# Kernel optimization log

Measured on AMD Instinct MI355X. Metric: run time of the kernel, lower is better.

Reference implementation:

```python
import jax, jax.numpy as jnp
import numpy as np

B, S, T = 256, 1024, 128

def setup_inputs() -> dict:
    key = jax.random.key(0)
    k1, k2, k3, k4, k5 = jax.random.split(key, 5)
    return {
        "emissions": jax.random.normal(k1, (B, S, T), dtype=jnp.float32),
        "tags": jax.random.randint(k2, (B, S), 0, T, dtype=jnp.int64 if jax.config.jax_enable_x64 else jnp.int32),
        "mask": jnp.ones((B, S), dtype=jnp.float32),
        "start_transitions": jax.random.normal(k3, (T,), dtype=jnp.float32),
        "end_transitions": jax.random.normal(k4, (T,), dtype=jnp.float32),
        "transitions": jax.random.normal(k5, (T, T), dtype=jnp.float32),
    }


def _gold_score(emissions, tags, mask, start_transitions, end_transitions, transitions):
    # score of the gold tag sequence (note: original uses log_softmax'd emissions here)
    score = start_transitions[tags[:, 0]]
    logp = jax.nn.log_softmax(emissions, axis=2)
    em_sc = jnp.take_along_axis(logp, tags[:, :, None], axis=2)[:, :, 0] * mask  # [B,S]
    score = score + em_sc.sum(axis=1)
    trans_sc = transitions[tags[:, :-1], tags[:, 1:]] * mask[:, 1:]  # [B,S-1]
    score = score + trans_sc.sum(axis=1)
    score = score + end_transitions[tags[:, -1]] * mask[:, -1]
    return score


def _forward_score(emissions, mask, start_transitions, end_transitions, transitions):
    # partition function via forward algorithm (faithful to original, incl. its
    # masking quirk: alpha recurrence is unmasked; only the last step's masked
    # alpha is used for the final logsumexp)
    alpha0 = start_transitions + emissions[:, 0]  # [B,T]

    def step(carry, inp):
        alpha, _ = carry
        em_t, m_t = inp  # [B,T], [B]
        # [B,T_prev,T_cur] broadcast add, logsumexp over prev tag
        new_alpha = jax.nn.logsumexp(
            alpha[:, :, None] + transitions[None, :, :] + em_t[:, None, :], axis=1
        )
        return (new_alpha, new_alpha * m_t[:, None]), None

    xs = (jnp.swapaxes(emissions[:, 1:], 0, 1), jnp.swapaxes(mask[:, 1:], 0, 1))
    (_, alpha_masked), _ = jax.lax.scan(step, (alpha0, jnp.zeros_like(alpha0)), xs)
    return jax.nn.logsumexp(alpha_masked + end_transitions, axis=1)  # [B]


def reference(emissions, tags, mask, start_transitions, end_transitions, transitions):
    score = _gold_score(emissions, tags, mask, start_transitions, end_transitions, transitions)
    fwd = _forward_score(emissions, mask, start_transitions, end_transitions, transitions)
    return jnp.mean(fwd - score)
```

## Files before the change

kernel.cpp:

```cpp
#include <hip/hip_runtime.h>

#define CRF_B 256
#define CRF_S 1024
#define CRF_T 128
#define GSPLIT 8
#define NFWD   CRF_B
#define NGOLD  (CRF_B * GSPLIT)
#define WS_FWD (CRF_B * GSPLIT)
#define WS_N   (WS_FWD + CRF_B)

typedef __attribute__((ext_vector_type(4))) float f32x4;

__device__ __forceinline__ void barrier_lds_only() {
    __asm__ volatile("s_waitcnt lgkmcnt(0)\n\ts_barrier" ::: "memory");
}

__device__ __forceinline__ float dpp_add_xor1(float x) {
    int y = __builtin_amdgcn_mov_dpp(__float_as_int(x), 0xB1, 0xF, 0xF, false);
    return x + __int_as_float(y);
}
__device__ __forceinline__ float dpp_add_xor2(float x) {
    int y = __builtin_amdgcn_mov_dpp(__float_as_int(x), 0x4E, 0xF, 0xF, false);
    return x + __int_as_float(y);
}

__device__ __forceinline__ f32x4 exp4(f32x4 v) {
    f32x4 r;
    r.x = __expf(v.x); r.y = __expf(v.y); r.z = __expf(v.z); r.w = __expf(v.w);
    return r;
}
__device__ __forceinline__ float hsum4(f32x4 v) {
    return (v.x + v.y) + (v.z + v.w);
}

__device__ __forceinline__ void fwd_block(
    const int b, const int tid,
    const float* __restrict__ em, const float* __restrict__ mask,
    const float* __restrict__ startT, const float* __restrict__ endT,
    const float* __restrict__ trans, float* __restrict__ ws)
{
    const int r  = tid & 3;
    const int cq = tid >> 2;
    const int j0 = cq * 4;
    const bool leader = (r == 0);

    __shared__ __align__(16) float Abuf[2][CRF_T];
    __shared__ __align__(16) float partsA[32];
    __shared__ float red[4];
    __shared__ float lzsh;

    int kidx[8];
#pragma unroll
    for (int k = 0; k < 8; ++k) kidx[k] = (k + 2 * r) & 7;

    f32x4 EE[8][4];
#pragma unroll
    for (int k = 0; k < 8; ++k) {
#pragma unroll
        for (int s = 0; s < 4; ++s) {
            const int i = 32 * r + 4 * kidx[k] + s;
            f32x4 t4 = *(const f32x4*)&trans[i * CRF_T + j0];
            EE[k][0][s] = __expf(t4.x);
            EE[k][1][s] = __expf(t4.y);
            EE[k][2][s] = __expf(t4.z);
            EE[k][3][s] = __expf(t4.w);
        }
    }

    const float* emb = em + (size_t)b * CRF_S * CRF_T + j0;
    const float mlast = mask[(size_t)b * CRF_S + (CRF_S - 1)];

    float logZ = 0.f;
    float rc = 1.f;

    f32x4 emv[4], eh[2][4];
#pragma unroll
    for (int k = 0; k < 4; ++k) emv[k] = *(const f32x4*)(emb + (size_t)k * CRF_T);
#pragma unroll
    for (int k = 0; k < 4; ++k) eh[0][k] = exp4(emv[k]);
#pragma unroll
    for (int k = 0; k < 4; ++k) emv[k] = *(const f32x4*)(emb + (size_t)(4 + k) * CRF_T);

    auto STEP = [&](int t, int role, f32x4 ehv) {
        const int rb = (t & 1) ^ 1, wb = t & 1;

        if (role == 3 && leader && t < 1023) {
            const f32x4* pa = (const f32x4*)partsA;
            f32x4 s8 = ((pa[0] + pa[1]) + (pa[2] + pa[3])) +
                       ((pa[4] + pa[5]) + (pa[6] + pa[7]));
            float c = hsum4(s8);
            rc = __builtin_amdgcn_rcpf(c);
            logZ += __logf(c);
        }

        const f32x4* A4 = (const f32x4*)&Abuf[rb][32 * r];
        f32x4 av = A4[kidx[0]];
        f32x4 ac0 = av * EE[0][0];
        f32x4 ac1 = av * EE[0][1];
        f32x4 ac2 = av * EE[0][2];
        f32x4 ac3 = av * EE[0][3];
#pragma unroll
        for (int k = 1; k < 8; ++k) {
            av = A4[kidx[k]];
            ac0 = __builtin_elementwise_fma(av, EE[k][0], ac0);
            ac1 = __builtin_elementwise_fma(av, EE[k][1], ac1);
            ac2 = __builtin_elementwise_fma(av, EE[k][2], ac2);
            ac3 = __builtin_elementwise_fma(av, EE[k][3], ac3);
        }
        float d0 = hsum4(ac0), d1 = hsum4(ac1), d2 = hsum4(ac2), d3 = hsum4(ac3);
        d0 = dpp_add_xor2(dpp_add_xor1(d0));
        d1 = dpp_add_xor2(dpp_add_xor1(d1));
        d2 = dpp_add_xor2(dpp_add_xor1(d2));
        d3 = dpp_add_xor2(dpp_add_xor1(d3));

        float a0 = d0 * ehv.x, a1 = d1 * ehv.y, a2 = d2 * ehv.z, a3 = d3 * ehv.w;
        if (role == 0) { a0 *= rc; a1 *= rc; a2 *= rc; a3 *= rc; }
        if (leader) {
            f32x4 avw = {a0, a1, a2, a3};
            *(f32x4*)&Abuf[wb][j0] = avw;
            if (role == 2) partsA[cq] = (a0 + a1) + (a2 + a3);
        }
        barrier_lds_only();
    };

    {
        f32x4 s4 = *(const f32x4*)&startT[j0];
        if (leader) {
            f32x4 a;
            a.x = __expf(s4.x) * eh[0][0].x;
            a.y = __expf(s4.y) * eh[0][0].y;
            a.z = __expf(s4.z) * eh[0][0].z;
            a.w = __expf(s4.w) * eh[0][0].w;
            *(f32x4*)&Abuf[0][j0] = a;
        }
        barrier_lds_only();
        STEP(1, 1, eh[0][1]);
#pragma unroll
        for (int k = 0; k < 4; ++k) eh[1][k] = exp4(emv[k]);
        STEP(2, 2, eh[0][2]);
#pragma unroll
        for (int k = 0; k < 4; ++k) emv[k] = *(const f32x4*)(emb + (size_t)(8 + k) * CRF_T);
        STEP(3, 3, eh[0][3]);
    }

#pragma unroll 1
    for (int g = 1; g < 256; ++g) {
        const int t0 = 4 * g;
        const int cur = g & 1, nxt = cur ^ 1;
        STEP(t0 + 0, 0, eh[cur][0]);
        STEP(t0 + 1, 1, eh[cur][1]);
        if (g <= 254) {
#pragma unroll
            for (int k = 0; k < 4; ++k) eh[nxt][k] = exp4(emv[k]);
        }
        STEP(t0 + 2, 2, eh[cur][2]);
        if (g <= 253) {
#pragma unroll
            for (int k = 0; k < 4; ++k)
                emv[k] = *(const f32x4*)(emb + (size_t)(t0 + 8 + k) * CRF_T);
        }
        STEP(t0 + 3, 3, eh[cur][3]);
    }

    __syncthreads();
    if (tid == 0) lzsh = logZ;
    __syncthreads();
    const float lz = lzsh;

    float v = (__logf(Abuf[1][tid]) + lz) * mlast + endT[tid];
    float mx = v;
#pragma unroll
    for (int dd = 1; dd < 64; dd <<= 1) mx = fmaxf(mx, __shfl_xor(mx, dd));
    if ((tid & 63) == 0) red[tid >> 6] = mx;
    __syncthreads();
    mx = fmaxf(red[0], red[1]);
    float ex = __expf(v - mx);
#pragma unroll
    for (int dd = 1; dd < 64; dd <<= 1) ex += __shfl_xor(ex, dd);
    if ((tid & 63) == 0) red[2 + (tid >> 6)] = ex;
    __syncthreads();
    if (tid == 0)
        ws[WS_FWD + b] = mx + __logf(red[2] + red[3]);
}

__device__ __forceinline__ void gold_block(
    const int gb, const int tid,
    const float* __restrict__ em, const int* __restrict__ tags,
    const float* __restrict__ mask, const float* __restrict__ startT,
    const float* __restrict__ endT, const float* __restrict__ trans,
    float* __restrict__ ws)
{
    const int b     = gb >> 3;
    const int slice = gb & (GSPLIT - 1);
    const int base  = slice << 7;
    const int p = tid & 3;
    const int q = tid >> 2;
    const int* tg = tags + (size_t)b * CRF_S;
    const float* mk = mask + (size_t)b * CRF_S;
    const float* emr = em + (size_t)b * CRF_S * CRF_T;

    __shared__ float r2g[2];

    float g_acc = 0.f;
    {
        const int t = base + tid;
        const int tagt = tg[t];
        const float m = mk[t];
        g_acc += emr[(size_t)t * CRF_T + tagt] * m;
        if (t >= 1) g_acc += trans[tg[t - 1] * CRF_T + tagt] * m;
    }
    if (tid == 0 && slice == 0)
        g_acc += startT[tg[0]];
    if (tid == 0 && slice == GSPLIT - 1)
        g_acc += endT[tg[CRF_S - 1]] * mk[CRF_S - 1];

    float s2 = 0.f;
#pragma unroll
    for (int it = 0; it < 4; ++it) {
        const int rr = base + it * 32 + q;
        const float* row = emr + (size_t)rr * CRF_T;
        f32x4 sum4 = {0.f, 0.f, 0.f, 0.f};
#pragma unroll
        for (int k = 0; k < 8; ++k)
            sum4 += exp4(*(const f32x4*)(row + k * 16 + p * 4));
        float s = hsum4(sum4);
        s = dpp_add_xor1(s);
        s = dpp_add_xor2(s);
        if (p == 0) s2 += __logf(s) * mk[rr];
    }

    float contrib = s2 - g_acc;
#pragma unroll
    for (int d = 1; d < 64; d <<= 1) contrib += __shfl_xor(contrib, d);
    if ((tid & 63) == 0) r2g[tid >> 6] = contrib;
    __syncthreads();
    if (tid == 0)
        ws[gb] = r2g[0] + r2g[1];
}

__global__ __launch_bounds__(128, 1) void crf_main_kernel(
    const float* __restrict__ em, const int* __restrict__ tags,
    const float* __restrict__ mask, const float* __restrict__ startT,
    const float* __restrict__ endT, const float* __restrict__ trans,
    float* __restrict__ ws)
{
    if (blockIdx.x < NFWD)
        fwd_block(blockIdx.x, threadIdx.x, em, mask, startT, endT, trans, ws);
    else
        gold_block(blockIdx.x - NFWD, threadIdx.x, em, tags, mask, startT,
                   endT, trans, ws);
}

__global__ __launch_bounds__(256) void crf_reduce_kernel(
    const float* __restrict__ ws, float* __restrict__ out)
{
    const int tid = threadIdx.x;
    float s = 0.f;
#pragma unroll
    for (int k = 0; k < WS_N; k += 256) s += ws[k + tid];
#pragma unroll
    for (int d = 1; d < 64; d <<= 1) s += __shfl_xor(s, d);
    __shared__ float r4[4];
    if ((tid & 63) == 0) r4[tid >> 6] = s;
    __syncthreads();
    if (tid == 0)
        out[0] = ((r4[0] + r4[1]) + (r4[2] + r4[3])) * (1.0f / CRF_B);
}

extern "C" void kernel_launch(void* const* d_in, const int* in_sizes, int n_in,
                              void* d_out, int out_size, void* d_ws, size_t ws_size,
                              hipStream_t stream)
{
    const float* em     = (const float*)d_in[0];
    const int*   tags   = (const int*)d_in[1];
    const float* mask   = (const float*)d_in[2];
    const float* startT = (const float*)d_in[3];
    const float* endT   = (const float*)d_in[4];
    const float* trans  = (const float*)d_in[5];
    float* out = (float*)d_out;
    float* ws  = (float*)d_ws;

    hipLaunchKernelGGL(crf_main_kernel, dim3(NFWD + NGOLD), dim3(128), 0, stream,
                       em, tags, mask, startT, endT, trans, ws);
    hipLaunchKernelGGL(crf_reduce_kernel, dim3(1), dim3(256), 0, stream,
                       ws, out);
}
```

Measured before the change: 597.1 us.

## Run CRF forward recurrence in a single wave, replacing barriers with permlane swaps

The forward-algorithm block now uses only one 64-lane wavefront instead of two. Each half-wave covers 64 of the 128 previous tags and combines its partial sums with permlane32_swap, so the per-step s_barrier is gone. The normalizer is recomputed by every lane from the LDS alpha vector, and the final logsumexp stays in registers without shared reductions. The cost is twice as many exp-transition registers per thread (16x4 f32x4) and more FMA work per lane, which puts register pressure and occupancy at risk. Correctness also depends on LDS ordering within one wave without explicit barriers.

```diff
diff --git a/kernel.cpp b/kernel.cpp
--- a/kernel.cpp
+++ b/kernel.cpp
@@ -11,8 +11,14 @@
 
 typedef __attribute__((ext_vector_type(4))) float f32x4;
 
-__device__ __forceinline__ void barrier_lds_only() {
-    __asm__ volatile("s_waitcnt lgkmcnt(0)\n\ts_barrier" ::: "memory");
+__device__ __forceinline__ void wait_lds() {
+    __asm__ volatile("s_waitcnt lgkmcnt(0)" ::: "memory");
+}
+
+__device__ __forceinline__ float xhalf_sum(float x) {
+    int xi = __float_as_int(x);
+    auto r = __builtin_amdgcn_permlane32_swap(xi, xi, false, false);
+    return __int_as_float(r[0]) + __int_as_float(r[1]);
 }
 
 __device__ __forceinline__ float dpp_add_xor1(float x) {
@@ -39,31 +45,23 @@
     const float* __restrict__ startT, const float* __restrict__ endT,
     const float* __restrict__ trans, float* __restrict__ ws)
 {
-    const int r  = tid & 3;
-    const int cq = tid >> 2;
-    const int j0 = cq * 4;
-    const bool leader = (r == 0);
-
-    __shared__ __align__(16) float Abuf[2][CRF_T];
-    __shared__ __align__(16) float partsA[32];
-    __shared__ float red[4];
-    __shared__ float lzsh;
-
-    int kidx[8];
-#pragma unroll
-    for (int k = 0; k < 8; ++k) kidx[k] = (k + 2 * r) & 7;
-
-    f32x4 EE[8][4];
-#pragma unroll
-    for (int k = 0; k < 8; ++k) {
+    __shared__ __align__(16) float Ab[2][CRF_T];
+
+    const int h  = tid >> 5;
+    const int c  = tid & 31;
+    const int j0 = 4 * c;
+
+    f32x4 EH[16][4];
+#pragma unroll
+    for (int k = 0; k < 16; ++k) {
 #pragma unroll
         for (int s = 0; s < 4; ++s) {
-            const int i = 32 * r + 4 * kidx[k] + s;
-            f32x4 t4 = *(const f32x4*)&trans[i * CRF_T + j0];
-            EE[k][0][s] = __expf(t4.x);
-            EE[k][1][s] = __expf(t4.y);
-            EE[k][2][s] = __expf(t4.z);
-            EE[k][3][s] = __expf(t4.w);
+            const int row = 64 * h + 4 * k + s;
+            f32x4 t4 = *(const f32x4*)&trans[row * CRF_T + j0];
+            EH[k][0][s] = __expf(t4.x);
+            EH[k][1][s] = __expf(t4.y);
+            EH[k][2][s] = __expf(t4.z);
+            EH[k][3][s] = __expf(t4.w);
         }
     }
 
@@ -72,6 +70,7 @@
 
     float logZ = 0.f;
     float rc = 1.f;
+    f32x4 aout = {0.f, 0.f, 0.f, 0.f};
 
     f32x4 emv[4], eh[2][4];
 #pragma unroll
@@ -84,56 +83,59 @@
     auto STEP = [&](int t, int role, f32x4 ehv) {
         const int rb = (t & 1) ^ 1, wb = t & 1;
 
-        if (role == 3 && leader && t < 1023) {
-            const f32x4* pa = (const f32x4*)partsA;
-            f32x4 s8 = ((pa[0] + pa[1]) + (pa[2] + pa[3])) +
-                       ((pa[4] + pa[5]) + (pa[6] + pa[7]));
-            float c = hsum4(s8);
-            rc = __builtin_amdgcn_rcpf(c);
-            logZ += __logf(c);
-        }
-
-        const f32x4* A4 = (const f32x4*)&Abuf[rb][32 * r];
-        f32x4 av = A4[kidx[0]];
-        f32x4 ac0 = av * EE[0][0];
-        f32x4 ac1 = av * EE[0][1];
-        f32x4 ac2 = av * EE[0][2];
-        f32x4 ac3 = av * EE[0][3];
-#pragma unroll
-        for (int k = 1; k < 8; ++k) {
-            av = A4[kidx[k]];
-            ac0 = __builtin_elementwise_fma(av, EE[k][0], ac0);
-            ac1 = __builtin_elementwise_fma(av, EE[k][1], ac1);
-            ac2 = __builtin_elementwise_fma(av, EE[k][2], ac2);
-            ac3 = __builtin_elementwise_fma(av, EE[k][3], ac3);
-        }
-        float d0 = hsum4(ac0), d1 = hsum4(ac1), d2 = hsum4(ac2), d3 = hsum4(ac3);
-        d0 = dpp_add_xor2(dpp_add_xor1(d0));
-        d1 = dpp_add_xor2(dpp_add_xor1(d1));
-        d2 = dpp_add_xor2(dpp_add_xor1(d2));
-        d3 = dpp_add_xor2(dpp_add_xor1(d3));
-
-        float a0 = d0 * ehv.x, a1 = d1 * ehv.y, a2 = d2 * ehv.z, a3 = d3 * ehv.w;
-        if (role == 0) { a0 *= rc; a1 *= rc; a2 *= rc; a3 *= rc; }
-        if (leader) {
-            f32x4 avw = {a0, a1, a2, a3};
-            *(f32x4*)&Abuf[wb][j0] = avw;
-            if (role == 2) partsA[cq] = (a0 + a1) + (a2 + a3);
-        }
-        barrier_lds_only();
+        wait_lds();
+
+        const f32x4* A4 = (const f32x4*)&Ab[rb][64 * h];
+        f32x4 av[16];
+#pragma unroll
+        for (int k = 0; k < 16; ++k) av[k] = A4[k];
+
+        if (role == 3 && t < 1023) {
+            f32x4 cs = ((av[0] + av[1]) + (av[2] + av[3])) +
+                       ((av[4] + av[5]) + (av[6] + av[7]));
+            cs += ((av[8] + av[9]) + (av[10] + av[11])) +
+                  ((av[12] + av[13]) + (av[14] + av[15]));
+            float ch = hsum4(cs);
+            float cfull = xhalf_sum(ch);
+            rc = __builtin_amdgcn_rcpf(cfull);
+            logZ += __logf(cfull);
+        }
+
+        f32x4 ac0 = av[0] * EH[0][0];
+        f32x4 ac1 = av[0] * EH[0][1];
+        f32x4 ac2 = av[0] * EH[0][2];
+        f32x4 ac3 = av[0] * EH[0][3];
+#pragma unroll
+        for (int k = 1; k < 16; ++k) {
+            ac0 = __builtin_elementwise_fma(av[k], EH[k][0], ac0);
+            ac1 = __builtin_elementwise_fma(av[k], EH[k][1], ac1);
+            ac2 = __builtin_elementwise_fma(av[k], EH[k][2], ac2);
+            ac3 = __builtin_elementwise_fma(av[k], EH[k][3], ac3);
+        }
+        float d0 = xhalf_sum(hsum4(ac0));
+        float d1 = xhalf_sum(hsum4(ac1));
+        float d2 = xhalf_sum(hsum4(ac2));
+        float d3 = xhalf_sum(hsum4(ac3));
+
+        f32x4 a4;
+        a4.x = d0 * ehv.x; a4.y = d1 * ehv.y;
+        a4.z = d2 * ehv.z; a4.w = d3 * ehv.w;
+        if (role == 0) { a4.x *= rc; a4.y *= rc; a4.z *= rc; a4.w *= rc; }
+        if (h == 0)
+            *(f32x4*)&Ab[wb][j0] = a4;
+        aout = a4;
     };
 
     {
         f32x4 s4 = *(const f32x4*)&startT[j0];
-        if (leader) {
-            f32x4 a;
-            a.x = __expf(s4.x) * eh[0][0].x;
-            a.y = __expf(s4.y) * eh[0][0].y;
-            a.z = __expf(s4.z) * eh[0][0].z;
-            a.w = __expf(s4.w) * eh[0][0].w;
-            *(f32x4*)&Abuf[0][j0] = a;
-        }
-        barrier_lds_only();
+        f32x4 a;
+        a.x = __expf(s4.x) * eh[0][0].x;
+        a.y = __expf(s4.y) * eh[0][0].y;
+        a.z = __expf(s4.z) * eh[0][0].z;
+        a.w = __expf(s4.w) * eh[0][0].w;
+        if (h == 0)
+            *(f32x4*)&Ab[0][j0] = a;
+        aout = a;
         STEP(1, 1, eh[0][1]);
 #pragma unroll
         for (int k = 0; k < 4; ++k) eh[1][k] = exp4(emv[k]);
@@ -162,25 +164,22 @@
         STEP(t0 + 3, 3, eh[cur][3]);
     }
 
-    __syncthreads();
-    if (tid == 0) lzsh = logZ;
-    __syncthreads();
-    const float lz = lzsh;
-
-    float v = (__logf(Abuf[1][tid]) + lz) * mlast + endT[tid];
-    float mx = v;
-#pragma unroll
-    for (int dd = 1; dd < 64; dd <<= 1) mx = fmaxf(mx, __shfl_xor(mx, dd));
-    if ((tid & 63) == 0) red[tid >> 6] = mx;
-    __syncthreads();
-    mx = fmaxf(red[0], red[1]);
-    float ex = __expf(v - mx);
-#pragma unroll
-    for (int dd = 1; dd < 64; dd <<= 1) ex += __shfl_xor(ex, dd);
-    if ((tid & 63) == 0) red[2 + (tid >> 6)] = ex;
-    __syncthreads();
+    f32x4 v4;
+    v4.x = (__logf(aout.x) + logZ) * mlast + endT[j0 + 0];
+    v4.y = (__logf(aout.y) + logZ) * mlast + endT[j0 + 1];
+    v4.z = (__logf(aout.z) + logZ) * mlast + endT[j0 + 2];
+    v4.w = (__logf(aout.w) + logZ) * mlast + endT[j0 + 3];
+    float mx = fmaxf(fmaxf(v4.x, v4.y), fmaxf(v4.z, v4.w));
+#pragma unroll
+    for (int d = 1; d < 64; d <<= 1) mx = fmaxf(mx, __shfl_xor(mx, d));
+    float ex = 0.f;
+    if (h == 0)
+        ex = __expf(v4.x - mx) + __expf(v4.y - mx) +
+             __expf(v4.z - mx) + __expf(v4.w - mx);
+#pragma unroll
+    for (int d = 1; d < 64; d <<= 1) ex += __shfl_xor(ex, d);
     if (tid == 0)
-        ws[WS_FWD + b] = mx + __logf(red[2] + red[3]);
+        ws[WS_FWD + b] = mx + __logf(ex);
 }
 
 __device__ __forceinline__ void gold_block(
@@ -244,11 +243,13 @@
     const float* __restrict__ endT, const float* __restrict__ trans,
     float* __restrict__ ws)
 {
-    if (blockIdx.x < NFWD)
+    if (blockIdx.x < NFWD) {
+        if (threadIdx.x >= 64) return;
         fwd_block(blockIdx.x, threadIdx.x, em, mask, startT, endT, trans, ws);
-    else
+    } else {
         gold_block(blockIdx.x - NFWD, threadIdx.x, em, tags, mask, startT,
                    endT, trans, ws);
+    }
 }
 
 __global__ __launch_bounds__(256) void crf_reduce_kernel(
```

Result: slower. 1.088 ms (+82.2%).

## Widen CRF blocks to 256 threads and fuse final reduction via atomic counter

Applied to the files above, without the earlier changes.

The forward recurrence now spreads each column's reduction over previous tags across 8 lanes instead of 4. That halves the per-thread FMA chain on the serial critical path, at the cost of one extra DPP reduction stage. The four LDS reads for a step are issued first, before the prefetch and exp work, to hide their latency. The separate reduce kernel is removed: the last block, found by an atomic counter, does the final sum, with a memset to reset the counter. Gold blocks are adapted to 256 threads. The wider blocks give each CU more active waves but also more barrier participants per step.

```diff
diff --git a/kernel.cpp b/kernel.cpp
--- a/kernel.cpp
+++ b/kernel.cpp
@@ -6,6 +6,7 @@
 #define GSPLIT 8
 #define NFWD   CRF_B
 #define NGOLD  (CRF_B * GSPLIT)
+#define NBLK   (NFWD + NGOLD)
 #define WS_FWD (CRF_B * GSPLIT)
 #define WS_N   (WS_FWD + CRF_B)
 
@@ -21,6 +22,10 @@
 }
 __device__ __forceinline__ float dpp_add_xor2(float x) {
     int y = __builtin_amdgcn_mov_dpp(__float_as_int(x), 0x4E, 0xF, 0xF, false);
+    return x + __int_as_float(y);
+}
+__device__ __forceinline__ float dpp_add_xor4u(float x) {
+    int y = __builtin_amdgcn_mov_dpp(__float_as_int(x), 0x141, 0xF, 0xF, false);
     return x + __int_as_float(y);
 }
 
@@ -39,26 +44,26 @@
     const float* __restrict__ startT, const float* __restrict__ endT,
     const float* __restrict__ trans, float* __restrict__ ws)
 {
-    const int r  = tid & 3;
-    const int cq = tid >> 2;
+    const int r = tid & 7;
+    const int cq = tid >> 3;
     const int j0 = cq * 4;
     const bool leader = (r == 0);
 
     __shared__ __align__(16) float Abuf[2][CRF_T];
     __shared__ __align__(16) float partsA[32];
-    __shared__ float red[4];
+    __shared__ float red[8];
     __shared__ float lzsh;
 
-    int kidx[8];
-#pragma unroll
-    for (int k = 0; k < 8; ++k) kidx[k] = (k + 2 * r) & 7;
-
-    f32x4 EE[8][4];
-#pragma unroll
-    for (int k = 0; k < 8; ++k) {
+    int kidx[4];
+#pragma unroll
+    for (int k = 0; k < 4; ++k) kidx[k] = (k + r) & 3;
+
+    f32x4 EE[4][4];
+#pragma unroll
+    for (int k = 0; k < 4; ++k) {
 #pragma unroll
         for (int s = 0; s < 4; ++s) {
-            const int i = 32 * r + 4 * kidx[k] + s;
+            const int i = r * 16 + kidx[k] * 4 + s;
             f32x4 t4 = *(const f32x4*)&trans[i * CRF_T + j0];
             EE[k][0][s] = __expf(t4.x);
             EE[k][1][s] = __expf(t4.y);
@@ -81,8 +86,15 @@
 #pragma unroll
     for (int k = 0; k < 4; ++k) emv[k] = *(const f32x4*)(emb + (size_t)(4 + k) * CRF_T);
 
-    auto STEP = [&](int t, int role, f32x4 ehv) {
+    auto STEP = [&](int t, int role, f32x4 ehv, auto&& filler) {
         const int rb = (t & 1) ^ 1, wb = t & 1;
+
+        const f32x4* A4 = (const f32x4*)&Abuf[rb][r * 16];
+        f32x4 av[4];
+#pragma unroll
+        for (int k = 0; k < 4; ++k) av[k] = A4[kidx[k]];
+
+        filler();
 
         if (role == 3 && leader && t < 1023) {
             const f32x4* pa = (const f32x4*)partsA;
@@ -93,25 +105,22 @@
             logZ += __logf(c);
         }
 
-        const f32x4* A4 = (const f32x4*)&Abuf[rb][32 * r];
-        f32x4 av = A4[kidx[0]];
-        f32x4 ac0 = av * EE[0][0];
-        f32x4 ac1 = av * EE[0][1];
-        f32x4 ac2 = av * EE[0][2];
-        f32x4 ac3 = av * EE[0][3];
-#pragma unroll
-        for (int k = 1; k < 8; ++k) {
-            av = A4[kidx[k]];
-            ac0 = __builtin_elementwise_fma(av, EE[k][0], ac0);
-            ac1 = __builtin_elementwise_fma(av, EE[k][1], ac1);
-            ac2 = __builtin_elementwise_fma(av, EE[k][2], ac2);
-            ac3 = __builtin_elementwise_fma(av, EE[k][3], ac3);
+        f32x4 ac0 = av[0] * EE[0][0];
+        f32x4 ac1 = av[0] * EE[0][1];
+        f32x4 ac2 = av[0] * EE[0][2];
+        f32x4 ac3 = av[0] * EE[0][3];
+#pragma unroll
+        for (int k = 1; k < 4; ++k) {
+            ac0 = __builtin_elementwise_fma(av[k], EE[k][0], ac0);
+            ac1 = __builtin_elementwise_fma(av[k], EE[k][1], ac1);
+            ac2 = __builtin_elementwise_fma(av[k], EE[k][2], ac2);
+            ac3 = __builtin_elementwise_fma(av[k], EE[k][3], ac3);
         }
         float d0 = hsum4(ac0), d1 = hsum4(ac1), d2 = hsum4(ac2), d3 = hsum4(ac3);
-        d0 = dpp_add_xor2(dpp_add_xor1(d0));
-        d1 = dpp_add_xor2(dpp_add_xor1(d1));
-        d2 = dpp_add_xor2(dpp_add_xor1(d2));
-        d3 = dpp_add_xor2(dpp_add_xor1(d3));
+        d0 = dpp_add_xor4u(dpp_add_xor2(dpp_add_xor1(d0)));
+        d1 = dpp_add_xor4u(dpp_add_xor2(dpp_add_xor1(d1)));
+        d2 = dpp_add_xor4u(dpp_add_xor2(dpp_add_xor1(d2)));
+        d3 = dpp_add_xor4u(dpp_add_xor2(dpp_add_xor1(d3)));
 
         float a0 = d0 * ehv.x, a1 = d1 * ehv.y, a2 = d2 * ehv.z, a3 = d3 * ehv.w;
         if (role == 0) { a0 *= rc; a1 *= rc; a2 *= rc; a3 *= rc; }
@@ -122,6 +131,8 @@
         }
         barrier_lds_only();
     };
+
+    auto NOFILL = [] {};
 
     {
         f32x4 s4 = *(const f32x4*)&startT[j0];
@@ -134,32 +145,37 @@
             *(f32x4*)&Abuf[0][j0] = a;
         }
         barrier_lds_only();
-        STEP(1, 1, eh[0][1]);
-#pragma unroll
-        for (int k = 0; k < 4; ++k) eh[1][k] = exp4(emv[k]);
-        STEP(2, 2, eh[0][2]);
-#pragma unroll
-        for (int k = 0; k < 4; ++k) emv[k] = *(const f32x4*)(emb + (size_t)(8 + k) * CRF_T);
-        STEP(3, 3, eh[0][3]);
+        STEP(1, 1, eh[0][1], NOFILL);
+        STEP(2, 2, eh[0][2], [&] {
+#pragma unroll
+            for (int k = 0; k < 4; ++k) eh[1][k] = exp4(emv[k]);
+        });
+        STEP(3, 3, eh[0][3], [&] {
+#pragma unroll
+            for (int k = 0; k < 4; ++k)
+                emv[k] = *(const f32x4*)(emb + (size_t)(8 + k) * CRF_T);
+        });
     }
 
 #pragma unroll 1
     for (int g = 1; g < 256; ++g) {
         const int t0 = 4 * g;
         const int cur = g & 1, nxt = cur ^ 1;
-        STEP(t0 + 0, 0, eh[cur][0]);
-        STEP(t0 + 1, 1, eh[cur][1]);
-        if (g <= 254) {
-#pragma unroll
-            for (int k = 0; k < 4; ++k) eh[nxt][k] = exp4(emv[k]);
-        }
-        STEP(t0 + 2, 2, eh[cur][2]);
-        if (g <= 253) {
-#pragma unroll
-            for (int k = 0; k < 4; ++k)
-                emv[k] = *(const f32x4*)(emb + (size_t)(t0 + 8 + k) * CRF_T);
-        }
-        STEP(t0 + 3, 3, eh[cur][3]);
+        STEP(t0 + 0, 0, eh[cur][0], NOFILL);
+        STEP(t0 + 1, 1, eh[cur][1], NOFILL);
+        STEP(t0 + 2, 2, eh[cur][2], [&] {
+            if (g <= 254) {
+#pragma unroll
+                for (int k = 0; k < 4; ++k) eh[nxt][k] = exp4(emv[k]);
+            }
+        });
+        STEP(t0 + 3, 3, eh[cur][3], [&] {
+            if (g <= 253) {
+#pragma unroll
+                for (int k = 0; k < 4; ++k)
+                    emv[k] = *(const f32x4*)(emb + (size_t)(t0 + 8 + k) * CRF_T);
+            }
+        });
     }
 
     __syncthreads();
@@ -167,20 +183,22 @@
     __syncthreads();
     const float lz = lzsh;
 
-    float v = (__logf(Abuf[1][tid]) + lz) * mlast + endT[tid];
+    float v = -3.0e38f;
+    if (tid < 128)
+        v = (__logf(Abuf[1][tid]) + lz) * mlast + endT[tid];
     float mx = v;
 #pragma unroll
     for (int dd = 1; dd < 64; dd <<= 1) mx = fmaxf(mx, __shfl_xor(mx, dd));
     if ((tid & 63) == 0) red[tid >> 6] = mx;
     __syncthreads();
-    mx = fmaxf(red[0], red[1]);
-    float ex = __expf(v - mx);
+    mx = fmaxf(fmaxf(red[0], red[1]), fmaxf(red[2], red[3]));
+    float ex = (tid < 128) ? __expf(v - mx) : 0.f;
 #pragma unroll
     for (int dd = 1; dd < 64; dd <<= 1) ex += __shfl_xor(ex, dd);
-    if ((tid & 63) == 0) red[2 + (tid >> 6)] = ex;
+    if ((tid & 63) == 0) red[4 + (tid >> 6)] = ex;
     __syncthreads();
     if (tid == 0)
-        ws[WS_FWD + b] = mx + __logf(red[2] + red[3]);
+        ws[WS_FWD + b] = mx + __logf((red[4] + red[5]) + (red[6] + red[7]));
 }
 
 __device__ __forceinline__ void gold_block(
@@ -199,10 +217,10 @@
     const float* mk = mask + (size_t)b * CRF_S;
     const float* emr = em + (size_t)b * CRF_S * CRF_T;
 
-    __shared__ float r2g[2];
+    __shared__ float r4g[4];
 
     float g_acc = 0.f;
-    {
+    if (tid < 128) {
         const int t = base + tid;
         const int tagt = tg[t];
         const float m = mk[t];
@@ -216,8 +234,8 @@
 
     float s2 = 0.f;
 #pragma unroll
-    for (int it = 0; it < 4; ++it) {
-        const int rr = base + it * 32 + q;
+    for (int it = 0; it < 2; ++it) {
+        const int rr = base + it * 64 + q;
         const float* row = emr + (size_t)rr * CRF_T;
         f32x4 sum4 = {0.f, 0.f, 0.f, 0.f};
 #pragma unroll
@@ -232,39 +250,47 @@
     float contrib = s2 - g_acc;
 #pragma unroll
     for (int d = 1; d < 64; d <<= 1) contrib += __shfl_xor(contrib, d);
-    if ((tid & 63) == 0) r2g[tid >> 6] = contrib;
+    if ((tid & 63) == 0) r4g[tid >> 6] = contrib;
     __syncthreads();
     if (tid == 0)
-        ws[gb] = r2g[0] + r2g[1];
-}
-
-__global__ __launch_bounds__(128, 1) void crf_main_kernel(
+        ws[gb] = (r4g[0] + r4g[1]) + (r4g[2] + r4g[3]);
+}
+
+__device__ __forceinline__ void finish_and_reduce(
+    float* __restrict__ ws, float* __restrict__ out, const int tid)
+{
+    __shared__ unsigned osh;
+    __shared__ float r4f[4];
+    __threadfence();
+    if (tid == 0)
+        osh = atomicAdd((unsigned*)(ws + WS_N), 1u);
+    __syncthreads();
+    if (osh != (unsigned)(NBLK - 1)) return;
+    __threadfence();
+
+    float s = 0.f;
+#pragma unroll
+    for (int k = 0; k < WS_N; k += 256) s += ws[k + tid];
+#pragma unroll
+    for (int d = 1; d < 64; d <<= 1) s += __shfl_xor(s, d);
+    if ((tid & 63) == 0) r4f[tid >> 6] = s;
+    __syncthreads();
+    if (tid == 0)
+        out[0] = ((r4f[0] + r4f[1]) + (r4f[2] + r4f[3])) * (1.0f / CRF_B);
+}
+
+__global__ __launch_bounds__(256) void crf_main_kernel(
     const float* __restrict__ em, const int* __restrict__ tags,
     const float* __restrict__ mask, const float* __restrict__ startT,
     const float* __restrict__ endT, const float* __restrict__ trans,
-    float* __restrict__ ws)
+    float* __restrict__ ws, float* __restrict__ out)
 {
     if (blockIdx.x < NFWD)
         fwd_block(blockIdx.x, threadIdx.x, em, mask, startT, endT, trans, ws);
     else
         gold_block(blockIdx.x - NFWD, threadIdx.x, em, tags, mask, startT,
                    endT, trans, ws);
-}
-
-__global__ __launch_bounds__(256) void crf_reduce_kernel(
-    const float* __restrict__ ws, float* __restrict__ out)
-{
-    const int tid = threadIdx.x;
-    float s = 0.f;
-#pragma unroll
-    for (int k = 0; k < WS_N; k += 256) s += ws[k + tid];
-#pragma unroll
-    for (int d = 1; d < 64; d <<= 1) s += __shfl_xor(s, d);
-    __shared__ float r4[4];
-    if ((tid & 63) == 0) r4[tid >> 6] = s;
-    __syncthreads();
-    if (tid == 0)
-        out[0] = ((r4[0] + r4[1]) + (r4[2] + r4[3])) * (1.0f / CRF_B);
+    finish_and_reduce(ws, out, threadIdx.x);
 }
 
 extern "C" void kernel_launch(void* const* d_in, const int* in_sizes, int n_in,
@@ -280,8 +306,7 @@
     float* out = (float*)d_out;
     float* ws  = (float*)d_ws;
 
-    hipLaunchKernelGGL(crf_main_kernel, dim3(NFWD + NGOLD), dim3(128), 0, stream,
-                       em, tags, mask, startT, endT, trans, ws);
-    hipLaunchKernelGGL(crf_reduce_kernel, dim3(1), dim3(256), 0, stream,
-                       ws, out);
-}
+    hipMemsetAsync((void*)(ws + WS_N), 0, sizeof(unsigned), stream);
+    hipLaunchKernelGGL(crf_main_kernel, dim3(NBLK), dim3(256), 0, stream,
+                       em, tags, mask, startT, endT, trans, ws, out);
+}
```

Result: slower. 689.2 us (+15.4%).
